# Kernel tuning notes

Hardware: AMD Instinct MI355X
Metric: run time of the kernel (lower is better)

Reference implementation:

```python
import jax, jax.numpy as jnp
import numpy as np

T, B, H = 512, 64, 1024

def setup_inputs() -> dict:
    key = jax.random.key(0)
    ks = jax.random.split(key, 16)
    names_mat = ['W_ir', 'W_hr', 'W_iz', 'W_hz', 'W_in', 'W_hn']
    names_vec = ['b_ir', 'b_hr', 'b_iz', 'b_hz', 'b_in', 'b_hn']
    inp = {
        'input_': jax.random.normal(ks[0], (T, B, H), dtype=jnp.float32),
        'hidden0': jax.random.normal(ks[1], (B, H), dtype=jnp.float32),
    }
    for i, n in enumerate(names_mat):
        inp[n] = jax.random.normal(ks[2 + i], (H, H), dtype=jnp.float32)
    for i, n in enumerate(names_vec):
        inp[n] = jax.random.normal(ks[8 + i], (H,), dtype=jnp.float32)
    # W = randn(H) * T, b = randn(1) in the original forward; made explicit here
    inp['W_out'] = jax.random.normal(ks[14], (H,), dtype=jnp.float32) * T
    inp['b_out'] = jax.random.normal(ks[15], (1,), dtype=jnp.float32)
    return inp

def reference(input_, hidden0, W_ir, W_hr, W_iz, W_hz, W_in, W_hn,
              b_ir, b_hr, b_iz, b_hz, b_in, b_hn, W_out, b_out):
    h = input_.shape[2]
    # permutation matrix is identity -> lower = tril(ones)
    lower = jnp.tril(jnp.ones((h, h), dtype=input_.dtype))
    Wir, Whr = W_ir * lower, W_hr * lower
    Wiz, Whz = W_iz * lower, W_hz * lower
    Win, Whn = W_in * lower, W_hn * lower

    def step(hid, x):
        # mask == x in the original call: cell(x, lower, x, hidden)
        r = jax.nn.sigmoid(x @ Wir + b_ir * x + hid @ Whr + b_hr)
        z = jax.nn.sigmoid(x @ Wiz + b_iz * x + hid @ Whz + b_hz)
        n = jnp.tanh(x @ Win + b_in * x + r * (hid @ Whn + b_hn))
        hid_new = hid * z + (1.0 - z) * n
        label = jax.nn.sigmoid(hid_new * W_out + b_out) * x  # [B, H]
        return hid_new, label

    _, labels = jax.lax.scan(step, hidden0, input_)  # labels: [T, B, H]
    ans_f = jnp.max(labels, axis=-1)                 # [T, B]
    ans = jnp.where(ans_f >= 0.5, 1, -1).astype(jnp.int32)
    return ans
```

## Files before the change

kernel.cpp:

```cpp
#include <hip/hip_runtime.h>

#define T_DIM 512
#define B_DIM 64
#define H_DIM 1024
#define KSLOT 33
#define APITCH 1032
#define AHEAD 6

typedef __attribute__((ext_vector_type(8))) short bf16x8;
typedef __attribute__((ext_vector_type(4))) float f32x4;


__device__ __forceinline__ unsigned short f2bf(float f) {
    unsigned u = __float_as_uint(f);
    unsigned r = (u + 0x7FFFu + ((u >> 16) & 1u)) >> 16;
    return (unsigned short)r;
}
__device__ __forceinline__ unsigned pack2(float a, float b) {
    return (unsigned)f2bf(a) | ((unsigned)f2bf(b) << 16);
}

__global__ __launch_bounds__(128) void prep_pack(
    const float* __restrict__ Wir, const float* __restrict__ Wiz, const float* __restrict__ Win,
    const float* __restrict__ Whr, const float* __restrict__ Whz, const float* __restrict__ Whn,
    unsigned short* __restrict__ Wpk)
{
    const float* srcs[6] = {Wir, Wiz, Win, Whr, Whz, Whn};
    const int t    = threadIdx.x;
    const int jtks = blockIdx.x;
    const int g    = blockIdx.y;
    const int jt   = jtks >> 5, ks = jtks & 31;
    const int lane = t >> 1, e0 = (t & 1) * 4;
    const float* src = srcs[g];
    const int j  = jt * 16 + (lane & 15);
    const int kb = ks * 32 + (lane >> 4) * 8 + e0;
    ushort4 o; unsigned short* po = (unsigned short*)&o;
    #pragma unroll
    for (int i = 0; i < 4; ++i) {
        const int k = kb + i;
        const float w = (k >= j) ? src[(size_t)k * H_DIM + j] : 0.0f;
        po[i] = f2bf(w);
    }
    const size_t idx = ((((size_t)jt * KSLOT + ks) * 6 + g) * 64 + lane) * 8 + e0;
    *(ushort4*)(Wpk + idx) = o;
}

__global__ __launch_bounds__(256) void init_h(const float* __restrict__ h0,
                                              unsigned short* __restrict__ hring,
                                              unsigned* __restrict__ prog)
{
    if (blockIdx.x < 256) {
        const int i = blockIdx.x * 256 + threadIdx.x;
        hring[i] = f2bf(h0[i]);
    } else {
        #pragma unroll
        for (int k = 0; k < 16; ++k) prog[threadIdx.x + 256 * k] = 0u;
    }
}

__global__ __launch_bounds__(512) void gru_main(
    const float* __restrict__ x,
    const unsigned short* __restrict__ Wpk,
    const float* __restrict__ bir, const float* __restrict__ bhr,
    const float* __restrict__ biz, const float* __restrict__ bhz,
    const float* __restrict__ bin_, const float* __restrict__ bhn,
    const float* __restrict__ Wout, const float* __restrict__ bout,
    const float* __restrict__ h0,
    unsigned short* __restrict__ hring,
    float* __restrict__ pmax,
    unsigned* __restrict__ prog)
{
    __shared__ __align__(16) unsigned short axf[16 * APITCH];
    __shared__ __align__(16) unsigned short ahf[16 * APITCH];
    __shared__ float red[8][6][64][4];
    __shared__ float hown[16][17];
    __shared__ unsigned short hb[16][16];

    const int tid  = threadIdx.x;
    const int lane = tid & 63;
    const int wv   = tid >> 6;

    const int jt = blockIdx.x & 63;
    const int bg = blockIdx.x >> 6;
    const int b0 = bg * 16;

    const int ksb   = jt >> 1;
    const int kcol0 = ksb * 32;
    const int CHN   = (H_DIM - kcol0) >> 3;
    const int cnt   = 32 - ksb;
    const int kpw   = (cnt + 7) >> 3;
    const int ks_s  = ksb + wv * kpw;
    const int ks_e  = (ks_s + kpw < 32) ? (ks_s + kpw) : 32;

    const int row = lane & 15;
    const int kg  = lane >> 4;
    const unsigned short* pax = &axf[row * APITCH + kg * 8];
    const unsigned short* pah = &ahf[row * APITCH + kg * 8];
    const unsigned short* pw0 = Wpk + (size_t)jt * KSLOT * 3072 + lane * 8;

    const int ecol = tid & 15;
    const int eb   = tid >> 4;
    const int ej   = 16 * jt + ecol;
    float c_bir = 0, c_bhr = 0, c_biz = 0, c_bhz = 0, c_bin = 0, c_bhn = 0, c_wo = 0, bo = 0;
    if (tid < 256) {
        c_bir = bir[ej]; c_bhr = bhr[ej]; c_biz = biz[ej]; c_bhz = bhz[ej];
        c_bin = bin_[ej]; c_bhn = bhn[ej]; c_wo = Wout[ej]; bo = bout[0];
    }

    unsigned* myflag = prog + ((bg << 6) + jt) * 16;
    unsigned* pollp  = prog + ((bg << 6) + lane) * 16;

    if (tid < 256) hown[eb][ecol] = h0[(size_t)(b0 + eb) * H_DIM + ej];
    #pragma unroll
    for (int rr = 0; rr < 2; ++rr) {
        const int r = 2 * wv + rr;
        const float* src = x + (size_t)(b0 + r) * H_DIM + kcol0;
        #pragma unroll
        for (int s = 0; s < 2; ++s) {
            const int c8 = lane + (s << 6);
            if (c8 < CHN) {
                const float4 v0 = *(const float4*)(src + c8 * 8);
                const float4 v1 = *(const float4*)(src + c8 * 8 + 4);
                uint4 o = make_uint4(pack2(v0.x, v0.y), pack2(v0.z, v0.w),
                                     pack2(v1.x, v1.y), pack2(v1.z, v1.w));
                *(uint4*)&axf[r * APITCH + c8 * 8] = o;
            }
        }
    }

    for (int t = 0; t < T_DIM; ++t) {
        const int slot_r = t & 7, slot_w = (t + 1) & 7;

        if (tid < 64) {
            const int kt = lane;
            int thr = -1000000;
            if (kt >= jt) thr = t;
            if (kt <= jt && t - AHEAD > thr) thr = t - AHEAD;
            for (;;) {
                const unsigned v = __hip_atomic_load(pollp, __ATOMIC_RELAXED,
                                                     __HIP_MEMORY_SCOPE_AGENT);
                if (__all((int)v >= thr)) break;
                __builtin_amdgcn_s_sleep(2);
            }
        }
        __syncthreads();

        #pragma unroll
        for (int rr = 0; rr < 2; ++rr) {
            const int r = 2 * wv + rr;
            const unsigned* src = (const unsigned*)(hring +
                ((size_t)slot_r * B_DIM + b0 + r) * H_DIM + kcol0);
            #pragma unroll
            for (int s = 0; s < 2; ++s) {
                const int c8 = lane + (s << 6);
                if (c8 < CHN) {
                    const unsigned* p4 = src + c8 * 4;
                    uint4 o;
                    o.x = __hip_atomic_load(p4 + 0, __ATOMIC_RELAXED, __HIP_MEMORY_SCOPE_AGENT);
                    o.y = __hip_atomic_load(p4 + 1, __ATOMIC_RELAXED, __HIP_MEMORY_SCOPE_AGENT);
                    o.z = __hip_atomic_load(p4 + 2, __ATOMIC_RELAXED, __HIP_MEMORY_SCOPE_AGENT);
                    o.w = __hip_atomic_load(p4 + 3, __ATOMIC_RELAXED, __HIP_MEMORY_SCOPE_AGENT);
                    *(uint4*)&ahf[r * APITCH + c8 * 8] = o;
                }
            }
        }
        __syncthreads();
        if (tid < 256) {
            const int kk = ((jt & 1) << 4) + ecol;
            ahf[eb * APITCH + kk] = f2bf(hown[eb][ecol]);
        }
        __syncthreads();

        f32x4 a0 = 0.f, a1 = 0.f, a2 = 0.f, a3 = 0.f, a4 = 0.f, a5 = 0.f;
        for (int ks = ks_s; ks < ks_e; ++ks) {
            const int off = (ks - ksb) * 32;
            const bf16x8 ax = *(const bf16x8*)(pax + off);
            const bf16x8 ah = *(const bf16x8*)(pah + off);
            const unsigned short* pw = pw0 + (size_t)ks * 3072;
            const bf16x8 w0 = *(const bf16x8*)(pw);
            const bf16x8 w1 = *(const bf16x8*)(pw + 512);
            const bf16x8 w2 = *(const bf16x8*)(pw + 1024);
            const bf16x8 w3 = *(const bf16x8*)(pw + 1536);
            const bf16x8 w4 = *(const bf16x8*)(pw + 2048);
            const bf16x8 w5 = *(const bf16x8*)(pw + 2560);
            a0 = __builtin_amdgcn_mfma_f32_16x16x32_bf16(ax, w0, a0, 0, 0, 0);
            a1 = __builtin_amdgcn_mfma_f32_16x16x32_bf16(ax, w1, a1, 0, 0, 0);
            a2 = __builtin_amdgcn_mfma_f32_16x16x32_bf16(ax, w2, a2, 0, 0, 0);
            a3 = __builtin_amdgcn_mfma_f32_16x16x32_bf16(ah, w3, a3, 0, 0, 0);
            a4 = __builtin_amdgcn_mfma_f32_16x16x32_bf16(ah, w4, a4, 0, 0, 0);
            a5 = __builtin_amdgcn_mfma_f32_16x16x32_bf16(ah, w5, a5, 0, 0, 0);
        }
        *(f32x4*)&red[wv][0][lane][0] = a0;
        *(f32x4*)&red[wv][1][lane][0] = a1;
        *(f32x4*)&red[wv][2][lane][0] = a2;
        *(f32x4*)&red[wv][3][lane][0] = a3;
        *(f32x4*)&red[wv][4][lane][0] = a4;
        *(f32x4*)&red[wv][5][lane][0] = a5;
        __syncthreads();

        if (tid < 256) {
            const int lp = ((eb >> 2) << 4) | ecol;
            const int rg = eb & 3;
            float s0 = 0, s1 = 0, s2 = 0, s3 = 0, s4 = 0, s5 = 0;
            #pragma unroll
            for (int w2i = 0; w2i < 8; ++w2i) {
                s0 += red[w2i][0][lp][rg]; s1 += red[w2i][1][lp][rg];
                s2 += red[w2i][2][lp][rg]; s3 += red[w2i][3][lp][rg];
                s4 += red[w2i][4][lp][rg]; s5 += red[w2i][5][lp][rg];
            }
            const float xv = x[(size_t)t * B_DIM * H_DIM + (size_t)(b0 + eb) * H_DIM + ej];
            const float hv = hown[eb][ecol];
            const float rp = s0 + c_bir * xv + c_bhr + s3;
            const float zp = s1 + c_biz * xv + c_bhz + s4;
            const float r  = 1.0f / (1.0f + expf(-rp));
            const float z  = 1.0f / (1.0f + expf(-zp));
            const float np = s2 + c_bin * xv + r * (s5 + c_bhn);
            const float n  = tanhf(np);
            const float hnew = hv * z + (1.0f - z) * n;
            hown[eb][ecol] = hnew;
            hb[eb][ecol] = f2bf(hnew);
            float lab = (1.0f / (1.0f + expf(-(hnew * c_wo + bo)))) * xv;
            #pragma unroll
            for (int off = 8; off; off >>= 1)
                lab = fmaxf(lab, __shfl_xor(lab, off));
            if (ecol == 0) pmax[((size_t)t * B_DIM + b0 + eb) * 64 + jt] = lab;
        }
        __syncthreads();

        if (tid < 128) {
            const int b = tid >> 3, cq = tid & 7;
            const unsigned val = (unsigned)hb[b][2 * cq] | ((unsigned)hb[b][2 * cq + 1] << 16);
            unsigned* dst = (unsigned*)(hring + ((size_t)slot_w * B_DIM + b0 + b) * H_DIM
                                        + 16 * jt) + cq;
            __hip_atomic_store(dst, val, __ATOMIC_RELAXED, __HIP_MEMORY_SCOPE_AGENT);
        }
        __syncthreads();
        if (tid == 0)
            __hip_atomic_store(myflag, (unsigned)(t + 1),
                               __ATOMIC_RELEASE, __HIP_MEMORY_SCOPE_AGENT);

        if (t < T_DIM - 1) {
            const float* xs = x + (size_t)(t + 1) * B_DIM * H_DIM;
            #pragma unroll
            for (int rr = 0; rr < 2; ++rr) {
                const int r = 2 * wv + rr;
                const float* src = xs + (size_t)(b0 + r) * H_DIM + kcol0;
                #pragma unroll
                for (int s = 0; s < 2; ++s) {
                    const int c8 = lane + (s << 6);
                    if (c8 < CHN) {
                        const float4 v0 = *(const float4*)(src + c8 * 8);
                        const float4 v1 = *(const float4*)(src + c8 * 8 + 4);
                        uint4 o = make_uint4(pack2(v0.x, v0.y), pack2(v0.z, v0.w),
                                             pack2(v1.x, v1.y), pack2(v1.z, v1.w));
                        *(uint4*)&axf[r * APITCH + c8 * 8] = o;
                    }
                }
            }
        }
    }
}

__global__ __launch_bounds__(256) void finalize(const float* __restrict__ pmax, int* __restrict__ out)
{
    const int i = blockIdx.x * 256 + threadIdx.x;
    if (i >= T_DIM * B_DIM) return;
    const float4* pm = (const float4*)(pmax + (size_t)i * 64);
    float m = -3.4e38f;
    #pragma unroll
    for (int q = 0; q < 16; ++q) {
        const float4 v = pm[q];
        m = fmaxf(m, fmaxf(fmaxf(v.x, v.y), fmaxf(v.z, v.w)));
    }
    out[i] = (m >= 0.5f) ? 1 : -1;
}

extern "C" void kernel_launch(void* const* d_in, const int* in_sizes, int n_in,
                              void* d_out, int out_size, void* d_ws, size_t ws_size,
                              hipStream_t stream)
{
    const float* x    = (const float*)d_in[0];
    const float* h0   = (const float*)d_in[1];
    const float* W_ir = (const float*)d_in[2];
    const float* W_hr = (const float*)d_in[3];
    const float* W_iz = (const float*)d_in[4];
    const float* W_hz = (const float*)d_in[5];
    const float* W_in = (const float*)d_in[6];
    const float* W_hn = (const float*)d_in[7];
    const float* b_ir = (const float*)d_in[8];
    const float* b_hr = (const float*)d_in[9];
    const float* b_iz = (const float*)d_in[10];
    const float* b_hz = (const float*)d_in[11];
    const float* b_in = (const float*)d_in[12];
    const float* b_hn = (const float*)d_in[13];
    const float* W_out = (const float*)d_in[14];
    const float* b_out = (const float*)d_in[15];

    unsigned short* Wpk   = (unsigned short*)d_ws;
    unsigned short* hring = Wpk + (size_t)64 * KSLOT * 3072;
    float* pmax = (float*)(hring + (size_t)8 * B_DIM * H_DIM);
    unsigned* prog = (unsigned*)(pmax + (size_t)T_DIM * B_DIM * 64);

    prep_pack<<<dim3(64 * 32, 6), 128, 0, stream>>>(W_ir, W_iz, W_in, W_hr, W_hz, W_hn, Wpk);
    init_h<<<dim3(257), 256, 0, stream>>>(h0, hring, prog);

    void* args[] = {(void*)&x, (void*)&Wpk,
                    (void*)&b_ir, (void*)&b_hr, (void*)&b_iz, (void*)&b_hz,
                    (void*)&b_in, (void*)&b_hn, (void*)&W_out, (void*)&b_out,
                    (void*)&h0, (void*)&hring, (void*)&pmax, (void*)&prog};
    hipError_t rc = hipLaunchCooperativeKernel((const void*)gru_main, dim3(256), dim3(512),
                                               args, 0, stream);
    (void)rc;

    finalize<<<dim3(T_DIM * B_DIM / 256), 256, 0, stream>>>(pmax, (int*)d_out);
}
```

Before: 6.087 ms.

## Streamline per-step GRU sync: cached flag polling, vector coherent loads, single-wave publish

The poll wave now caches the last observed flag values and skips the atomic poll when they already satisfy the thresholds. The own-column threshold is dropped, so the block no longer waits on itself. The hidden-state ring is read with four global_load_dwordx4 instructions carrying sc0 sc1 instead of sixteen scalar atomic loads, which also removes one barrier and the self-column overwrite. Publishing h and the release flag is folded into wave 0 with no barrier before it, while the other seven waves prefetch the next x slice concurrently. The aim is to shorten the serialized per-timestep critical path, at the cost of relying on hand-written inline asm for memory coherence and on the ring already holding the block's own columns.

```diff
diff --git a/kernel.cpp b/kernel.cpp
--- a/kernel.cpp
+++ b/kernel.cpp
@@ -128,46 +128,48 @@
         }
     }
 
+    unsigned cachedf = 0;
+
     for (int t = 0; t < T_DIM; ++t) {
         const int slot_r = t & 7, slot_w = (t + 1) & 7;
 
-        if (tid < 64) {
+        if (wv == 0) {
             const int kt = lane;
-            int thr = -1000000;
-            if (kt >= jt) thr = t;
-            if (kt <= jt && t - AHEAD > thr) thr = t - AHEAD;
-            for (;;) {
-                const unsigned v = __hip_atomic_load(pollp, __ATOMIC_RELAXED,
-                                                     __HIP_MEMORY_SCOPE_AGENT);
-                if (__all((int)v >= thr)) break;
-                __builtin_amdgcn_s_sleep(2);
+            int thr;
+            if (kt > jt) thr = t;
+            else if (kt < jt) thr = t - AHEAD;
+            else thr = -0x40000000;
+            if (!__all((int)cachedf >= thr)) {
+                for (;;) {
+                    cachedf = __hip_atomic_load(pollp, __ATOMIC_RELAXED,
+                                                __HIP_MEMORY_SCOPE_AGENT);
+                    if (__all((int)cachedf >= thr)) break;
+                    __builtin_amdgcn_s_sleep(2);
+                }
             }
         }
         __syncthreads();
 
-        #pragma unroll
-        for (int rr = 0; rr < 2; ++rr) {
-            const int r = 2 * wv + rr;
-            const unsigned* src = (const unsigned*)(hring +
-                ((size_t)slot_r * B_DIM + b0 + r) * H_DIM + kcol0);
-            #pragma unroll
-            for (int s = 0; s < 2; ++s) {
-                const int c8 = lane + (s << 6);
-                if (c8 < CHN) {
-                    const unsigned* p4 = src + c8 * 4;
-                    uint4 o;
-                    o.x = __hip_atomic_load(p4 + 0, __ATOMIC_RELAXED, __HIP_MEMORY_SCOPE_AGENT);
-                    o.y = __hip_atomic_load(p4 + 1, __ATOMIC_RELAXED, __HIP_MEMORY_SCOPE_AGENT);
-                    o.z = __hip_atomic_load(p4 + 2, __ATOMIC_RELAXED, __HIP_MEMORY_SCOPE_AGENT);
-                    o.w = __hip_atomic_load(p4 + 3, __ATOMIC_RELAXED, __HIP_MEMORY_SCOPE_AGENT);
-                    *(uint4*)&ahf[r * APITCH + c8 * 8] = o;
-                }
-            }
-        }
-        __syncthreads();
-        if (tid < 256) {
-            const int kk = ((jt & 1) << 4) + ecol;
-            ahf[eb * APITCH + kk] = f2bf(hown[eb][ecol]);
+        {
+            const unsigned short* base = hring + ((size_t)slot_r * B_DIM + b0) * H_DIM + kcol0;
+            const int r0 = 2 * wv, r1 = 2 * wv + 1;
+            const int cA = lane, cB = lane + 64;
+            const bool gB = (cB < CHN);
+            const bool gA = (cA < CHN);
+            uint4 o0, o1, o2, o3;
+            const unsigned short* a0 = base + (size_t)r0 * H_DIM + cA * 8;
+            const unsigned short* a1 = base + (size_t)r0 * H_DIM + cB * 8;
+            const unsigned short* a2 = base + (size_t)r1 * H_DIM + cA * 8;
+            const unsigned short* a3 = base + (size_t)r1 * H_DIM + cB * 8;
+            if (gA) asm volatile("global_load_dwordx4 %0, %1, off sc0 sc1" : "=v"(o0) : "v"(a0));
+            if (gB) asm volatile("global_load_dwordx4 %0, %1, off sc0 sc1" : "=v"(o1) : "v"(a1));
+            if (gA) asm volatile("global_load_dwordx4 %0, %1, off sc0 sc1" : "=v"(o2) : "v"(a2));
+            if (gB) asm volatile("global_load_dwordx4 %0, %1, off sc0 sc1" : "=v"(o3) : "v"(a3));
+            asm volatile("s_waitcnt vmcnt(0)" ::: "memory");
+            if (gA) *(uint4*)&ahf[r0 * APITCH + cA * 8] = o0;
+            if (gB) *(uint4*)&ahf[r0 * APITCH + cB * 8] = o1;
+            if (gA) *(uint4*)&ahf[r1 * APITCH + cA * 8] = o2;
+            if (gB) *(uint4*)&ahf[r1 * APITCH + cB * 8] = o3;
         }
         __syncthreads();
 
@@ -227,23 +229,23 @@
         }
         __syncthreads();
 
-        if (tid < 128) {
-            const int b = tid >> 3, cq = tid & 7;
-            const unsigned val = (unsigned)hb[b][2 * cq] | ((unsigned)hb[b][2 * cq + 1] << 16);
-            unsigned* dst = (unsigned*)(hring + ((size_t)slot_w * B_DIM + b0 + b) * H_DIM
-                                        + 16 * jt) + cq;
-            __hip_atomic_store(dst, val, __ATOMIC_RELAXED, __HIP_MEMORY_SCOPE_AGENT);
-        }
-        __syncthreads();
-        if (tid == 0)
-            __hip_atomic_store(myflag, (unsigned)(t + 1),
-                               __ATOMIC_RELEASE, __HIP_MEMORY_SCOPE_AGENT);
-
-        if (t < T_DIM - 1) {
+        if (wv == 0) {
+            #pragma unroll
+            for (int pp = 0; pp < 2; ++pp) {
+                const int i = lane + (pp << 6);
+                const int b = i >> 3, cq = i & 7;
+                const unsigned val = (unsigned)hb[b][2 * cq]
+                                   | ((unsigned)hb[b][2 * cq + 1] << 16);
+                unsigned* dst = (unsigned*)(hring +
+                    ((size_t)slot_w * B_DIM + b0 + b) * H_DIM + 16 * jt) + cq;
+                __hip_atomic_store(dst, val, __ATOMIC_RELAXED, __HIP_MEMORY_SCOPE_AGENT);
+            }
+            if (lane == 0)
+                __hip_atomic_store(myflag, (unsigned)(t + 1),
+                                   __ATOMIC_RELEASE, __HIP_MEMORY_SCOPE_AGENT);
+        } else if (t < T_DIM - 1) {
             const float* xs = x + (size_t)(t + 1) * B_DIM * H_DIM;
-            #pragma unroll
-            for (int rr = 0; rr < 2; ++rr) {
-                const int r = 2 * wv + rr;
+            for (int r = wv - 1; r < 16; r += 7) {
                 const float* src = xs + (size_t)(b0 + r) * H_DIM + kcol0;
                 #pragma unroll
                 for (int s = 0; s < 2; ++s) {
```

Measured after the change: 6.404 ms. 5.2% more time.
